# Kernel optimization log

Hardware: AMD Instinct MI355X
Metric: run time of the kernel (lower is better)

The kernel has to match this reference:

```python
import jax, jax.numpy as jnp
import numpy as np

N_FEATURES = 256
RAND_RANGE = 100.0


def _random_embed(x):
    """Deterministic pseudo-random embedding: each scalar in x seeds a counter-based
    RNG producing N_FEATURES uniforms in [0, RAND_RANGE). (JAX threefry replaces
    Python's Mersenne Twister; same structure: value-seeded deterministic uniforms.)"""
    flat = jax.lax.stop_gradient(x).reshape(-1)
    seeds = jax.lax.bitcast_convert_type(flat, jnp.uint32)  # value -> integer seed
    base = jax.random.key(42)
    keys = jax.vmap(lambda s: jax.random.fold_in(base, s))(seeds)
    emb = jax.vmap(lambda k: jax.random.uniform(k, (N_FEATURES,), minval=0.0, maxval=RAND_RANGE))(keys)
    return emb.reshape(x.shape + (N_FEATURES,))  # [B, S, F]


def setup_inputs() -> dict:
    key = jax.random.key(0)
    kx, kw, kb = jax.random.split(key, 3)
    x = jax.random.normal(kx, (256, 512), dtype=jnp.float32)
    W = jax.random.normal(kw, (N_FEATURES, N_FEATURES), dtype=jnp.float32) * 0.05
    b = jax.random.normal(kb, (N_FEATURES,), dtype=jnp.float32) * 0.05
    return {"x": x, "W": W, "b": b}


def reference(x, W, b):
    emb = _random_embed(x)                      # [B, S, F]
    out = jnp.einsum('bsf,gf->bsg', emb, W) + b  # nn.Linear: emb @ W.T + b
    return out
```

## Files before the change

### kernel.cpp

```cpp
#include <hip/hip_runtime.h>
#include <stdint.h>

#define F 256
#define R 64
#define THREADS 256
#define GCH 32
#define NCH (F / GCH)
#define CH_SLOTS (GCH * F / 8)

typedef __attribute__((ext_vector_type(8))) short short8;
typedef __attribute__((ext_vector_type(4))) float floatx4;

__device__ __forceinline__ uint32_t rotl32(uint32_t x, int d) {
  return __builtin_amdgcn_alignbit(x, x, (uint32_t)(32 - d));
}

struct TFK { uint32_t k0, k1, k2, a1, a2, a3, a4, a5; };

__device__ __forceinline__ TFK mkkeys(uint32_t k0, uint32_t k1) {
  TFK K;
  K.k0 = k0; K.k1 = k1; K.k2 = k0 ^ k1 ^ 0x1BD11BDAu;
  K.a1 = K.k2 + 1u; K.a2 = k0 + 2u; K.a3 = k1 + 3u;
  K.a4 = K.k2 + 4u; K.a5 = k0 + 5u;
  return K;
}

__device__ __forceinline__ void tf_one(const TFK& K, uint32_t& x0, uint32_t& x1) {
  x0 += K.k0; x1 += K.k1;
#define TF1(r) x0 += x1; x1 = rotl32(x1, r); x1 ^= x0;
  TF1(13) TF1(15) TF1(26) TF1(6)   x0 += K.k1; x1 += K.a1;
  TF1(17) TF1(29) TF1(16) TF1(24)  x0 += K.k2; x1 += K.a2;
  TF1(13) TF1(15) TF1(26) TF1(6)   x0 += K.k0; x1 += K.a3;
  TF1(17) TF1(29) TF1(16) TF1(24)  x0 += K.k1; x1 += K.a4;
  TF1(13) TF1(15) TF1(26) TF1(6)   x0 += K.k2; x1 += K.a5;
#undef TF1
}

__device__ __forceinline__ void tf_pair(const TFK& K, uint32_t i,
                                        uint32_t& oa, uint32_t& ob) {
  uint32_t a0 = K.k0, a1 = K.k1 + i;
  uint32_t b0 = K.k0, b1 = K.k1 + i + 1u;
#define TF2(r)  a0 += a1; b0 += b1;                         \
                a1 = rotl32(a1, r); b1 = rotl32(b1, r);     \
                a1 ^= a0; b1 ^= b0;
#define INJ2(u, v) a0 += (u); b0 += (u); a1 += (v); b1 += (v);
  TF2(13) TF2(15) TF2(26) TF2(6)   INJ2(K.k1, K.a1)
  TF2(17) TF2(29) TF2(16) TF2(24)  INJ2(K.k2, K.a2)
  TF2(13) TF2(15) TF2(26) TF2(6)   INJ2(K.k0, K.a3)
  TF2(17) TF2(29) TF2(16) TF2(24)  INJ2(K.k1, K.a4)
  TF2(13) TF2(15) TF2(26) TF2(6)   INJ2(K.k2, K.a5)
#undef TF2
#undef INJ2
  oa = a0 ^ a1;
  ob = b0 ^ b1;
}

__device__ __forceinline__ uint32_t featpack(const TFK& K, uint32_t i) {
  uint32_t xa, xb;
  tf_pair(K, i, xa, xb);
  uint32_t ulo = __float_as_uint((float)xa * 2.3283064365386963e-8f);
  uint32_t uhi = __float_as_uint((float)xb * 2.3283064365386963e-8f);
  ulo += 0x7FFFu + ((ulo >> 16) & 1u);
  uhi += 0x7FFFu + ((uhi >> 16) & 1u);
  return __builtin_amdgcn_perm(uhi, ulo, 0x07060302u);
}

__device__ __forceinline__ short8 quad(const TFK& K, uint32_t fb) {
  uint32_t w32[4];
  #pragma unroll
  for (int p = 0; p < 4; ++p) w32[p] = featpack(K, fb + 2u * p);
  union { uint32_t w[4]; short8 s; } u;
  u.w[0] = w32[0]; u.w[1] = w32[1]; u.w[2] = w32[2]; u.w[3] = w32[3];
  return u.s;
}

__device__ __forceinline__ uint32_t f2bf(float f) {
  uint32_t u = __float_as_uint(f);
  u += 0x7FFFu + ((u >> 16) & 1u);
  return u >> 16;
}

__global__ __launch_bounds__(256) void femb_conv(const float* __restrict__ W,
                                                 uint16_t* __restrict__ ws) {
  int s = blockIdx.x * 256 + threadIdx.x;
  int gt = s >> 10;
  int c = (s >> 5) & 31;
  int g = s & 31;
  const float4* src = (const float4*)(W + (size_t)(gt * GCH + g) * F + c * 8);
  float4 v0 = src[0], v1 = src[1];
  short8 o;
  o[0] = (short)f2bf(v0.x); o[1] = (short)f2bf(v0.y);
  o[2] = (short)f2bf(v0.z); o[3] = (short)f2bf(v0.w);
  o[4] = (short)f2bf(v1.x); o[5] = (short)f2bf(v1.y);
  o[6] = (short)f2bf(v1.z); o[7] = (short)f2bf(v1.w);
  *(short8*)(ws + (size_t)s * 8) = o;
}

__global__ __launch_bounds__(THREADS, 3) void femb_main(
    const float* __restrict__ x, const uint16_t* __restrict__ Wbf,
    const float* __restrict__ bias, float* __restrict__ out) {
  const int tid  = threadIdx.x;
  const int lane = tid & 63;
  const int wave = tid >> 6;
  const int qd   = lane >> 4;
  const int l16  = lane & 15;
  const size_t row0 = (size_t)blockIdx.x * R;
  const int myrow = (int)row0 + wave * 16 + l16;

  float xv = x[myrow];

  const TFK K42 = mkkeys(0u, 42u);
  uint32_t u0 = 0u, u1 = __float_as_uint(xv);
  tf_one(K42, u0, u1);
  const TFK K = mkkeys(u0, u1);

  short8 afragC = quad(K, (uint32_t)(qd * 8));

  const uint16_t* wlane = Wbf + (size_t)(qd * 256 + l16 * 8);

  floatx4 acc[16];
  #pragma unroll
  for (int n = 0; n < 16; ++n) acc[n] = (floatx4){0.f, 0.f, 0.f, 0.f};

  #pragma unroll 1
  for (int kt = 0; kt < NCH; ++kt) {
    const uint16_t* wk = wlane + (size_t)kt * 1024;
    const uint32_t fb = (uint32_t)((kt + 1) * GCH + qd * 8);
    const bool more = (kt + 1 < NCH);
    uint32_t w0 = 0, w1 = 0, w2 = 0, w3 = 0;
    short8 b[8];

    #pragma unroll
    for (int n = 0; n < 8; ++n)
      b[n] = *(const short8*)(wk + (n >> 1) * 8192 + (n & 1) * 128);
    if (more) { w0 = featpack(K, fb); w1 = featpack(K, fb + 2u); }
    #pragma unroll
    for (int n = 0; n < 8; ++n)
      acc[n] = __builtin_amdgcn_mfma_f32_16x16x32_bf16(afragC, b[n], acc[n],
                                                       0, 0, 0);

    #pragma unroll
    for (int n = 0; n < 8; ++n)
      b[n] = *(const short8*)(wk + ((n + 8) >> 1) * 8192 + (n & 1) * 128);
    if (more) { w2 = featpack(K, fb + 4u); w3 = featpack(K, fb + 6u); }
    #pragma unroll
    for (int n = 0; n < 8; ++n)
      acc[n + 8] = __builtin_amdgcn_mfma_f32_16x16x32_bf16(afragC, b[n],
                                                           acc[n + 8], 0, 0, 0);

    if (more) {
      union { uint32_t w[4]; short8 s; } u;
      u.w[0] = w0; u.w[1] = w1; u.w[2] = w2; u.w[3] = w3;
      afragC = u.s;
    }
  }

  const size_t growbase = row0 + (size_t)(wave * 16 + qd * 4);
  #pragma unroll
  for (int n = 0; n < 16; ++n) {
    int g = n * 16 + l16;
    float bg = bias[g];
    #pragma unroll
    for (int reg = 0; reg < 4; ++reg)
      out[(growbase + reg) * F + g] = acc[n][reg] + bg;
  }
}

extern "C" void kernel_launch(void* const* d_in, const int* in_sizes, int n_in,
                              void* d_out, int out_size, void* d_ws, size_t ws_size,
                              hipStream_t stream) {
  const float* x = (const float*)d_in[0];
  const float* W = (const float*)d_in[1];
  const float* b = (const float*)d_in[2];
  float* out = (float*)d_out;
  uint16_t* wsbf = (uint16_t*)d_ws;
  const int nrows = in_sizes[0];
  const int blocks = nrows / R;

  hipLaunchKernelGGL(femb_conv, dim3((F * F / 8) / 256), dim3(256), 0, stream, W, wsbf);
  hipLaunchKernelGGL(femb_main, dim3(blocks), dim3(THREADS), 0, stream,
                     x, wsbf, b, out);
}
```

Before: 214.3 us.

## Stage bf16 weight chunks through triple-buffered LDS via async global-to-LDS loads

The main kernel now streams the bf16 weight matrix into a three-slot LDS ring with global_load_lds DMA, prefetching two chunks ahead, and reads MFMA B operands from LDS instead of per-lane global loads. The loop order changes so that each chunk covers 32 output columns over all K. All 8 A fragments (the threefry embedding) are computed up front and held in registers, and the bias is preloaded. This is meant to hide global load latency and share weight loads across waves. In exchange it uses 48KB of LDS per block, adds block barriers, and raises register pressure, which may reduce occupancy below the requested 3 blocks.

```diff
diff --git a/kernel.cpp b/kernel.cpp
--- a/kernel.cpp
+++ b/kernel.cpp
@@ -7,6 +7,7 @@
 #define GCH 32
 #define NCH (F / GCH)
 #define CH_SLOTS (GCH * F / 8)
+#define NBUF 3
 
 typedef __attribute__((ext_vector_type(8))) short short8;
 typedef __attribute__((ext_vector_type(4))) float floatx4;
@@ -80,6 +81,21 @@
   return u >> 16;
 }
 
+__device__ __forceinline__ void gl_lds16(const void* gptr, void* lptr) {
+  __builtin_amdgcn_global_load_lds(
+      (const __attribute__((address_space(1))) uint32_t*)gptr,
+      (__attribute__((address_space(3))) uint32_t*)lptr, 16, 0, 0);
+}
+
+__device__ __forceinline__ void dma_chunk(const uint16_t* __restrict__ src,
+                                          uint16_t* dst, int wave, int lane) {
+  #pragma unroll
+  for (int it = 0; it < CH_SLOTS / THREADS; ++it) {
+    int sbase = it * THREADS + wave * 64;
+    gl_lds16(src + (size_t)(sbase + lane) * 8, dst + (size_t)sbase * 8);
+  }
+}
+
 __global__ __launch_bounds__(256) void femb_conv(const float* __restrict__ W,
                                                  uint16_t* __restrict__ ws) {
   int s = blockIdx.x * 256 + threadIdx.x;
@@ -99,6 +115,8 @@
 __global__ __launch_bounds__(THREADS, 3) void femb_main(
     const float* __restrict__ x, const uint16_t* __restrict__ Wbf,
     const float* __restrict__ bias, float* __restrict__ out) {
+  __shared__ uint16_t sW[NBUF][GCH * F];
+
   const int tid  = threadIdx.x;
   const int lane = tid & 63;
   const int wave = tid >> 6;
@@ -109,49 +127,51 @@
 
   float xv = x[myrow];
 
+  dma_chunk(Wbf, sW[0], wave, lane);
+  dma_chunk(Wbf + (size_t)CH_SLOTS * 8, sW[1], wave, lane);
+
+  float bgv[16];
+  #pragma unroll
+  for (int n = 0; n < 16; ++n) bgv[n] = bias[n * 16 + l16];
+
   const TFK K42 = mkkeys(0u, 42u);
   uint32_t u0 = 0u, u1 = __float_as_uint(xv);
   tf_one(K42, u0, u1);
   const TFK K = mkkeys(u0, u1);
 
-  short8 afragC = quad(K, (uint32_t)(qd * 8));
-
-  const uint16_t* wlane = Wbf + (size_t)(qd * 256 + l16 * 8);
+  short8 afrag[8];
+  #pragma unroll
+  for (int kt = 0; kt < 8; ++kt)
+    afrag[kt] = quad(K, (uint32_t)(kt * 32 + qd * 8));
 
   floatx4 acc[16];
   #pragma unroll
   for (int n = 0; n < 16; ++n) acc[n] = (floatx4){0.f, 0.f, 0.f, 0.f};
 
-  #pragma unroll 1
-  for (int kt = 0; kt < NCH; ++kt) {
-    const uint16_t* wk = wlane + (size_t)kt * 1024;
-    const uint32_t fb = (uint32_t)((kt + 1) * GCH + qd * 8);
-    const bool more = (kt + 1 < NCH);
-    uint32_t w0 = 0, w1 = 0, w2 = 0, w3 = 0;
-    short8 b[8];
-
+  #pragma unroll
+  for (int gt = 0; gt < NCH; ++gt) {
+    __builtin_amdgcn_sched_barrier(0);
+    if (gt == NCH - 1)
+      asm volatile("s_waitcnt vmcnt(0) lgkmcnt(0)" ::: "memory");
+    else
+      asm volatile("s_waitcnt vmcnt(4) lgkmcnt(0)" ::: "memory");
+    __builtin_amdgcn_s_barrier();
+    __builtin_amdgcn_sched_barrier(0);
+
+    if (gt + 2 < NCH)
+      dma_chunk(Wbf + (size_t)(gt + 2) * CH_SLOTS * 8,
+                sW[(gt + 2) % NBUF], wave, lane);
+
+    const uint16_t* buf = sW[gt % NBUF];
     #pragma unroll
-    for (int n = 0; n < 8; ++n)
-      b[n] = *(const short8*)(wk + (n >> 1) * 8192 + (n & 1) * 128);
-    if (more) { w0 = featpack(K, fb); w1 = featpack(K, fb + 2u); }
-    #pragma unroll
-    for (int n = 0; n < 8; ++n)
-      acc[n] = __builtin_amdgcn_mfma_f32_16x16x32_bf16(afragC, b[n], acc[n],
-                                                       0, 0, 0);
-
-    #pragma unroll
-    for (int n = 0; n < 8; ++n)
-      b[n] = *(const short8*)(wk + ((n + 8) >> 1) * 8192 + (n & 1) * 128);
-    if (more) { w2 = featpack(K, fb + 4u); w3 = featpack(K, fb + 6u); }
-    #pragma unroll
-    for (int n = 0; n < 8; ++n)
-      acc[n + 8] = __builtin_amdgcn_mfma_f32_16x16x32_bf16(afragC, b[n],
-                                                           acc[n + 8], 0, 0, 0);
-
-    if (more) {
-      union { uint32_t w[4]; short8 s; } u;
-      u.w[0] = w0; u.w[1] = w1; u.w[2] = w2; u.w[3] = w3;
-      afragC = u.s;
+    for (int kt = 0; kt < 8; ++kt) {
+      int c = kt * 4 + qd;
+      #pragma unroll
+      for (int n = 0; n < 2; ++n) {
+        short8 b = *(const short8*)&buf[(size_t)(c * 32 + n * 16 + l16) * 8];
+        acc[gt * 2 + n] = __builtin_amdgcn_mfma_f32_16x16x32_bf16(
+            afrag[kt], b, acc[gt * 2 + n], 0, 0, 0);
+      }
     }
   }
 
@@ -159,10 +179,9 @@
   #pragma unroll
   for (int n = 0; n < 16; ++n) {
     int g = n * 16 + l16;
-    float bg = bias[g];
     #pragma unroll
     for (int reg = 0; reg < 4; ++reg)
-      out[(growbase + reg) * F + g] = acc[n][reg] + bg;
+      out[(growbase + reg) * F + g] = acc[n][reg] + bgv[n];
   }
 }
 
```

Result: faster. 189.7 us (-11.5%).
